# Kernel optimization log

Hardware: AMD Instinct MI355X
Metric: run time of the kernel (lower is better)

Reference implementation:

```python
import jax, jax.numpy as jnp
import numpy as np

B, S, D, H, HD = 8, 1374, 384, 6, 64
NUM_PATCHES = 1369  # (518 // 14) ** 2
NUM_PREFIX = 5      # 1 cls + 4 registers


def setup_inputs() -> dict:
    key = jax.random.key(0)
    ks = jax.random.split(key, 10)
    init = 0.02  # truncated_normal(0.02) approximated by scaled normal
    x = jax.random.normal(ks[0], (B, S, D), jnp.float32)
    wq = jax.random.truncated_normal(ks[1], -2.0, 2.0, (D, H, HD), jnp.float32) * init
    wk = jax.random.truncated_normal(ks[2], -2.0, 2.0, (D, H, HD), jnp.float32) * init
    wv = jax.random.truncated_normal(ks[3], -2.0, 2.0, (D, H, HD), jnp.float32) * init
    wo = jax.random.truncated_normal(ks[4], -2.0, 2.0, (H, HD, D), jnp.float32) * init
    bq = jnp.zeros((H, HD), jnp.float32)
    bk = jnp.zeros((H, HD), jnp.float32)
    bv = jnp.zeros((H, HD), jnp.float32)
    bo = jnp.zeros((D,), jnp.float32)
    keep_patch_indices = jax.random.randint(ks[5], (B, NUM_PATCHES), 0, NUM_PATCHES).astype(jnp.int64)
    return {"x": x, "wq": wq, "bq": bq, "wk": wk, "bk": bk, "wv": wv, "bv": bv,
            "wo": wo, "bo": bo, "keep_patch_indices": keep_patch_indices, "k_patches": 685}


def reference(x, wq, bq, wk, bk, wv, bv, wo, bo, keep_patch_indices, k_patches):
    # q/k/v projections: DenseGeneral to (heads, head_dim)
    q = jnp.einsum('bsd,dhe->bshe', x, wq) + bq
    k = jnp.einsum('bsd,dhe->bshe', x, wk) + bk
    v = jnp.einsum('bsd,dhe->bshe', x, wv) + bv

    z = jnp.einsum('bqhd,bkhd->bhqk', q / (HD ** 0.5), k)  # [B,H,S,S]
    attn_logits = z  # saved BEFORE masking (used by 'mse' criterion)

    # dynamic scatter mask: patch columns >= k_patches get -inf
    num_selected = keep_patch_indices.shape[1]
    patch_idx = jnp.arange(num_selected)
    indices_to_mask = jnp.where(patch_idx >= k_patches, patch_idx, num_selected) + NUM_PREFIX
    # out-of-bounds indices (== num_selected + NUM_PREFIX) are dropped by JAX scatter semantics
    z = z.at[:, :, :, indices_to_mask].set(-jnp.inf)

    attn_map = jax.nn.softmax(z, axis=-1)
    zo = jnp.einsum('bhqk,bkhd->bqhd', attn_map, v)
    output = jnp.einsum('bqhd,hdo->bqo', zo, wo) + bo  # wo contracts (heads, head_dim)

    # attn_aggregate = ['cls_token','reg_token','patch_token'], zoom_map_criterion='mse'
    am = attn_logits.mean(axis=1)  # mean over heads -> [B,S,S]
    aggs = jnp.stack([
        am[:, 0:1, :].mean(axis=1),      # cls token
        am[:, 1:5, :].mean(axis=1),      # register tokens
        am[:, 5:1374, :].mean(axis=1),   # patch tokens
    ], axis=1)                            # [B,3,S]
    attn_agg = aggs.mean(axis=1)          # [B,S]
    return output, attn_agg
```

## Files before the change

### kernel.cpp

```cpp
#include <hip/hip_runtime.h>
#include <stdint.h>

#define BB 8
#define SS 1374
#define DD 384
#define HH 6
#define HDIM 64
#define MROWS (BB*SS)
#define NPFX 5
#define SPAD 1376

typedef __attribute__((ext_vector_type(8))) short bf16x8;
typedef __attribute__((ext_vector_type(4))) float f32x4;
typedef __attribute__((ext_vector_type(2))) unsigned int u32x2;
typedef __attribute__((ext_vector_type(4))) unsigned int u32x4;
typedef u32x4 __attribute__((aligned(4))) u32x4_u;

__device__ __forceinline__ unsigned short f2bf(float f){
  union { float f; unsigned int u; } v; v.f = f;
  return (unsigned short)((v.u + 0x7FFFu + ((v.u >> 16) & 1u)) >> 16);
}
__device__ __forceinline__ float bf2f(unsigned short b){
  union { float f; unsigned int u; } v; v.u = ((unsigned int)b) << 16; return v.f;
}
__device__ __forceinline__ unsigned int pk_bf16(float a, float b){
#if __has_builtin(__builtin_amdgcn_cvt_pk_bf16_f32)
  typedef __attribute__((ext_vector_type(2))) __bf16 bfv2;
  bfv2 p = __builtin_amdgcn_cvt_pk_bf16_f32(a, b);
  union { bfv2 v; unsigned int u; } c; c.v = p; return c.u;
#else
  return (unsigned int)f2bf(a) | ((unsigned int)f2bf(b) << 16);
#endif
}

__global__ void k_prep_x(const float* __restrict__ x, unsigned short* __restrict__ xb,
                         float* __restrict__ xbar){
  int b = blockIdx.x / 43, ch = blockIdx.x % 43;
  int d = threadIdx.x;
  int s0 = ch*32, s1 = s0 + 32; if (s1 > SS) s1 = SS;
  float acc = 0.f;
  for (int s = s0; s < s1; ++s){
    float v = x[((size_t)b*SS + s)*DD + d];
    float w = (s == 0) ? (1.f/3.f) : (s < 5) ? (1.f/12.f) : (1.f/4107.f);
    acc += w * v;
    xb[((size_t)b*SS + s)*DD + d] = f2bf(v);
  }
  atomicAdd(&xbar[b*DD + d], acc);
}

__global__ void k_conv_w(const float* __restrict__ wq, const float* __restrict__ wk,
                         const float* __restrict__ wv, const float* __restrict__ wo,
                         unsigned short* __restrict__ wbT, unsigned short* __restrict__ woT){
  int i = blockIdx.x*blockDim.x + threadIdx.x;
  if (i < 1152*384){
    int n = i / 384, d = i % 384;
    const float* w = (n < 384) ? wq : (n < 768) ? wk : wv;
    wbT[i] = f2bf(w[(size_t)d*384 + (n % 384)]);
  } else if (i < 1152*384 + 384*384){
    int j = i - 1152*384;
    int n = j / 384, k = j % 384;
    woT[j] = f2bf(wo[(size_t)k*384 + n]);
  }
}

__global__ void k_qbar(const float* __restrict__ xbar, const float* __restrict__ wq,
                       const float* __restrict__ bq, float* __restrict__ qbar){
  __shared__ float xs[DD];
  int b = blockIdx.x, t = threadIdx.x;
  xs[t] = xbar[b*DD + t];
  __syncthreads();
  float acc = bq[t];
  for (int d = 0; d < DD; ++d) acc += xs[d]*wq[(size_t)d*384 + t];
  qbar[b*384 + t] = acc;
}

__global__ void k_agg(const float* __restrict__ qbar, const unsigned short* __restrict__ kg,
                      float* __restrict__ out_agg){
  __shared__ float qs[384];
  int b = blockIdx.x / 6, sb = blockIdx.x % 6;
  int t = threadIdx.x;
  for (int i = t; i < 384; i += 256) qs[i] = qbar[b*384 + i];
  __syncthreads();
  int s = sb*256 + t;
  if (s >= SS) return;
  float acc = 0.f;
  for (int h = 0; h < HH; ++h){
    const unsigned short* kr = kg + (((size_t)(b*HH + h))*SS + s)*64;
    const float* qh = qs + h*64;
    for (int c = 0; c < 8; ++c){
      u32x4 v = *(const u32x4*)(kr + c*8);
      #pragma unroll
      for (int j = 0; j < 4; ++j){
        unsigned int u = v[j];
        acc += qh[c*8 + 2*j]     * bf2f((unsigned short)(u & 0xFFFFu));
        acc += qh[c*8 + 2*j + 1] * bf2f((unsigned short)(u >> 16));
      }
    }
  }
  out_agg[b*SS + s] = acc * (1.f/48.f);
}

template<int MODE>
__global__ __launch_bounds__(256) void k_gemm(
    const unsigned short* __restrict__ A, const unsigned short* __restrict__ Bt,
    const float* __restrict__ b0, const float* __restrict__ b1, const float* __restrict__ b2,
    unsigned short* __restrict__ qg, unsigned short* __restrict__ kgp,
    unsigned short* __restrict__ vt, float* __restrict__ out)
{
  int mt = blockIdx.x % 86, nt = blockIdx.x / 86;
  const int t = threadIdx.x;
  const int w = t >> 6, lane = t & 63, quad = lane >> 4, l16 = lane & 15;
  const int wm = w >> 1, wn = w & 1;
  constexpr int SMEM_SH = (MODE==0) ? 13824 : 17408;
  __shared__ unsigned short smem[SMEM_SH];
  unsigned short* As = smem;
  unsigned short* Bs = smem + 9216;
  f32x4 acc[4][2];
  #pragma unroll
  for (int i=0;i<4;i++){ acc[i][0] = (f32x4){0,0,0,0}; acc[i][1] = (f32x4){0,0,0,0}; }
  const int m0 = mt*128, n0 = nt*64;

  const int ar = t >> 1, akb = (t & 1) * 32;
  int ga = m0 + ar; if (ga > MROWS-1) ga = MROWS-1;
  const unsigned short* ap = A + (size_t)ga*384 + akb;
  const int br = t >> 2, bkb = (t & 3) * 16;
  const unsigned short* bp = Bt + (size_t)(n0 + br)*384 + bkb;

  u32x4 ra[4], rb[2];
  #pragma unroll
  for (int i=0;i<4;i++) ra[i] = *(const u32x4*)(ap + i*8);
  rb[0] = *(const u32x4*)(bp); rb[1] = *(const u32x4*)(bp + 8);

  for (int kc = 0; kc < 6; ++kc){
    __syncthreads();
    #pragma unroll
    for (int i=0;i<4;i++) *(u32x4*)(As + ar*72 + akb + i*8) = ra[i];
    *(u32x4*)(Bs + br*72 + bkb)     = rb[0];
    *(u32x4*)(Bs + br*72 + bkb + 8) = rb[1];
    __syncthreads();
    if (kc + 1 < 6){
      int kn = (kc+1)*64;
      #pragma unroll
      for (int i=0;i<4;i++) ra[i] = *(const u32x4*)(ap + kn + i*8);
      rb[0] = *(const u32x4*)(bp + kn); rb[1] = *(const u32x4*)(bp + kn + 8);
    }
    #pragma unroll
    for (int kh = 0; kh < 2; ++kh){
      bf16x8 af[4], bfr[2];
      #pragma unroll
      for (int rf = 0; rf < 4; ++rf)
        af[rf] = *(const bf16x8*)(As + (wm*64 + rf*16 + l16)*72 + kh*32 + quad*8);
      #pragma unroll
      for (int cf = 0; cf < 2; ++cf)
        bfr[cf] = *(const bf16x8*)(Bs + (wn*32 + cf*16 + l16)*72 + kh*32 + quad*8);
      #pragma unroll
      for (int rf = 0; rf < 4; ++rf)
        #pragma unroll
        for (int cf = 0; cf < 2; ++cf)
          acc[rf][cf] = __builtin_amdgcn_mfma_f32_16x16x32_bf16(af[rf], bfr[cf], acc[rf][cf], 0,0,0);
    }
  }

  const int b0r = m0 / SS, s0r = m0 % SS;
  __syncthreads();
  if (MODE == 1){
    float* CsF = (float*)smem;
    #pragma unroll
    for (int cf = 0; cf < 2; ++cf){
      int e = wn*32 + cf*16 + l16;
      float bias = b0[n0 + e];
      #pragma unroll
      for (int rf = 0; rf < 4; ++rf){
        int rr = wm*64 + rf*16 + quad*4;
        #pragma unroll
        for (int r4 = 0; r4 < 4; ++r4)
          CsF[(rr + r4)*68 + e] = acc[rf][cf][r4] + bias;
      }
    }
    __syncthreads();
    #pragma unroll
    for (int p = 0; p < 8; ++p){
      int r = p*16 + (t >> 4), c = t & 15;
      int rr = m0 + r;
      if (rr < MROWS){
        f32x4 v = *(const f32x4*)(CsF + r*68 + c*4);
        *(f32x4*)(out + (size_t)rr*384 + n0 + c*4) = v;
      }
    }
  } else {
    const int mat = nt / 6, h = nt - mat*6;
    const float* bvp = (mat==0) ? b0 : (mat==1) ? b1 : b2;
    const float vsc = (mat==0) ? 0.125f : 1.f;
    if (mat < 2){
      unsigned short* Cs = As;
      unsigned short* dst = (mat==0) ? qg : kgp;
      #pragma unroll
      for (int cf = 0; cf < 2; ++cf){
        int e = wn*32 + cf*16 + l16;
        float bias = bvp[h*64 + e];
        #pragma unroll
        for (int rf = 0; rf < 4; ++rf){
          int rr = wm*64 + rf*16 + quad*4;
          #pragma unroll
          for (int r4 = 0; r4 < 4; ++r4)
            Cs[(rr + r4)*72 + e] = f2bf((acc[rf][cf][r4] + bias)*vsc);
        }
      }
      __syncthreads();
      #pragma unroll
      for (int p = 0; p < 4; ++p){
        int r = p*32 + (t >> 3), c = t & 7;
        int rr = m0 + r;
        if (rr < MROWS){
          int s = s0r + r, bb = b0r;
          if (s >= SS){ s -= SS; ++bb; }
          u32x4 v = *(const u32x4*)(Cs + r*72 + c*8);
          *(u32x4*)(dst + (((size_t)(bb*HH + h))*SS + s)*64 + c*8) = v;
        }
      }
    } else {
      unsigned short* CsV = As;
      #pragma unroll
      for (int cf = 0; cf < 2; ++cf){
        int e = wn*32 + cf*16 + l16;
        float bias = bvp[h*64 + e];
        #pragma unroll
        for (int rf = 0; rf < 4; ++rf){
          int rr = wm*64 + rf*16 + quad*4;
          #pragma unroll
          for (int p = 0; p < 2; ++p)
            *(unsigned int*)(CsV + e*136 + rr + p*2) =
                pk_bf16(acc[rf][cf][p*2] + bias, acc[rf][cf][p*2+1] + bias);
        }
      }
      __syncthreads();
      const bool nowrap = (s0r + 127 < SS) && (m0 + 127 < MROWS);
      if (nowrap){
        int e = t >> 2;
        unsigned short* vrow = vt + ((size_t)(b0r*HH + h)*64 + e)*SPAD + s0r;
        #pragma unroll
        for (int i = 0; i < 4; ++i){
          int c = (t & 3)*4 + i;
          u32x4 v = *(const u32x4*)(CsV + e*136 + c*8);
          *(u32x4_u*)(vrow + c*8) = v;
        }
      } else {
        for (int idx = t; idx < 64*64; idx += 256){
          int e = idx >> 6, sp = (idx & 63)*2;
          int rr = m0 + sp;
          if (rr < MROWS){
            int s = s0r + sp, bb = b0r;
            if (s >= SS){ s -= SS; ++bb; }
            *(unsigned int*)(vt + ((size_t)(bb*HH + h)*64 + e)*SPAD + s) =
                *(const unsigned int*)(CsV + e*136 + sp);
          }
        }
      }
    }
  }
}

__global__ __launch_bounds__(128) void k_attn(
    const unsigned short* __restrict__ qg, const unsigned short* __restrict__ kg,
    const unsigned short* __restrict__ vt, unsigned short* __restrict__ zo,
    const int* __restrict__ kpat)
{
  int t = threadIdx.x, w = t >> 6, lane = t & 63, quad = lane >> 4, l16 = lane & 15;
  int wid = blockIdx.x*2 + w;
  int bh = wid / 43, qt = wid - bh*43;
  int q0 = qt*32;
  int SK = NPFX + kpat[0]; if (SK > SS) SK = SS; if (SK < 1) SK = 1;
  int niter = (SK + 63) >> 6;
  __shared__ unsigned short Ps[2][32*72];
  unsigned short* Pw = &Ps[w][0];
  const unsigned short* kbase = kg + ((size_t)bh*SS)*64;
  const unsigned short* vbase = vt + ((size_t)bh*64)*SPAD;

  bf16x8 aq[2][2];
  #pragma unroll
  for (int qf = 0; qf < 2; ++qf){
    int qrow = q0 + qf*16 + l16; if (qrow > SS-1) qrow = SS-1;
    const unsigned short* p = qg + ((size_t)bh*SS + qrow)*64;
    aq[qf][0] = *(const bf16x8*)(p + quad*8);
    aq[qf][1] = *(const bf16x8*)(p + 32 + quad*8);
  }
  f32x4 o[2][4];
  #pragma unroll
  for (int qf=0;qf<2;qf++)
    #pragma unroll
    for (int nc=0;nc<4;nc++) o[qf][nc] = (f32x4){0.f,0.f,0.f,0.f};
  float rsum[2][4] = {{0.f,0.f,0.f,0.f},{0.f,0.f,0.f,0.f}};

  auto loadK = [&](int k0, bf16x8 (&kf)[2][2][2]){
    #pragma unroll
    for (int ks = 0; ks < 2; ++ks)
      #pragma unroll
      for (int ns = 0; ns < 2; ++ns){
        const unsigned short* kr = kbase + (size_t)(k0 + ks*32 + 2*l16 + ns)*64;
        kf[ks][ns][0] = *(const bf16x8*)(kr + quad*8);
        kf[ks][ns][1] = *(const bf16x8*)(kr + 32 + quad*8);
      }
  };

  auto body = [&](int it, bf16x8 (&kfC)[2][2][2], bf16x8 (&kfN)[2][2][2]){
    int k0 = it*64;
    bf16x8 vf[2][4];
    #pragma unroll
    for (int kc = 0; kc < 2; ++kc)
      #pragma unroll
      for (int nc = 0; nc < 4; ++nc)
        vf[kc][nc] = *(const bf16x8*)(vbase + (size_t)(nc*16 + l16)*SPAD + k0 + kc*32 + quad*8);
    if (it + 1 < niter) loadK(k0 + 64, kfN);
    bool tail = (k0 + 64 > SK);
    #pragma unroll
    for (int ks = 0; ks < 2; ++ks){
      #pragma unroll
      for (int qf = 0; qf < 2; ++qf){
        float pp[2][4];
        #pragma unroll
        for (int ns = 0; ns < 2; ++ns){
          f32x4 zf = (f32x4){0.f,0.f,0.f,0.f};
          zf = __builtin_amdgcn_mfma_f32_16x16x32_bf16(aq[qf][0], kfC[ks][ns][0], zf, 0,0,0);
          zf = __builtin_amdgcn_mfma_f32_16x16x32_bf16(aq[qf][1], kfC[ks][ns][1], zf, 0,0,0);
          bool valid = !tail || (k0 + ks*32 + 2*l16 + ns) < SK;
          #pragma unroll
          for (int rg = 0; rg < 4; ++rg) pp[ns][rg] = valid ? __expf(zf[rg]) : 0.f;
        }
        #pragma unroll
        for (int rg = 0; rg < 4; ++rg){
          rsum[qf][rg] += pp[0][rg] + pp[1][rg];
          *(unsigned int*)(Pw + (qf*16 + quad*4 + rg)*72 + ks*32 + 2*l16) =
              pk_bf16(pp[0][rg], pp[1][rg]);
        }
      }
    }
    #pragma unroll
    for (int kc = 0; kc < 2; ++kc){
      bf16x8 ap0 = *(const bf16x8*)(Pw + l16*72        + kc*32 + quad*8);
      bf16x8 ap1 = *(const bf16x8*)(Pw + (16 + l16)*72 + kc*32 + quad*8);
      #pragma unroll
      for (int nc = 0; nc < 4; ++nc){
        o[0][nc] = __builtin_amdgcn_mfma_f32_16x16x32_bf16(ap0, vf[kc][nc], o[0][nc], 0,0,0);
        o[1][nc] = __builtin_amdgcn_mfma_f32_16x16x32_bf16(ap1, vf[kc][nc], o[1][nc], 0,0,0);
      }
    }
  };

  bf16x8 kfA[2][2][2], kfB[2][2][2];
  loadK(0, kfA);
  for (int it = 0; it < niter; it += 2){
    body(it, kfA, kfB);
    if (it + 1 < niter) body(it + 1, kfB, kfA);
  }

  int b = bh / HH, h = bh - (bh/HH)*HH;
  #pragma unroll
  for (int qf = 0; qf < 2; ++qf){
    #pragma unroll
    for (int rg = 0; rg < 4; ++rg){
      float s = rsum[qf][rg];
      #pragma unroll
      for (int off = 8; off >= 1; off >>= 1) s += __shfl_xor(s, off);
      int q = q0 + qf*16 + quad*4 + rg;
      if (q >= SS) continue;
      float inv = 1.f / s;
      unsigned short* dst = zo + ((size_t)b*SS + q)*384 + h*64;
      #pragma unroll
      for (int nc = 0; nc < 4; ++nc) dst[nc*16 + l16] = f2bf(o[qf][nc][rg]*inv);
    }
  }
}

extern "C" void kernel_launch(void* const* d_in, const int* in_sizes, int n_in,
                              void* d_out, int out_size, void* d_ws, size_t ws_size,
                              hipStream_t stream){
  const float* x  = (const float*)d_in[0];
  const float* wq = (const float*)d_in[1];
  const float* bq = (const float*)d_in[2];
  const float* wk = (const float*)d_in[3];
  const float* bk = (const float*)d_in[4];
  const float* wv = (const float*)d_in[5];
  const float* bv = (const float*)d_in[6];
  const float* wo = (const float*)d_in[7];
  const float* bo = (const float*)d_in[8];
  const int* kpat = (const int*)d_in[10];
  float* out = (float*)d_out;
  float* out_agg = out + (size_t)MROWS*DD;

  char* ws = (char*)d_ws;
  unsigned short* xb  = (unsigned short*)(ws);
  unsigned short* wbT = (unsigned short*)(ws +  8441856);
  unsigned short* woT = (unsigned short*)(ws +  9326592);
  unsigned short* qg  = (unsigned short*)(ws +  9621504);
  unsigned short* kg  = (unsigned short*)(ws + 18063360);
  unsigned short* vt  = (unsigned short*)(ws + 26505216);
  unsigned short* zo  = (unsigned short*)(ws + 34959360);
  float* xbar         = (float*)(ws + 43401216);
  float* qbar         = (float*)(ws + 43413504);
  (void)in_sizes; (void)n_in; (void)out_size; (void)ws_size;

  hipMemsetAsync(xbar, 0, BB*DD*sizeof(float), stream);
  k_prep_x<<<BB*43, DD, 0, stream>>>(x, xb, xbar);
  k_conv_w<<<((1152*384 + 384*384) + 255)/256, 256, 0, stream>>>(wq, wk, wv, wo, wbT, woT);
  k_qbar<<<BB, DD, 0, stream>>>(xbar, wq, bq, qbar);
  k_gemm<0><<<86*18, 256, 0, stream>>>(xb, wbT, bq, bk, bv, qg, kg, vt, nullptr);
  k_attn<<<1032, 128, 0, stream>>>(qg, kg, vt, zo, kpat);
  k_agg<<<BB*6, 256, 0, stream>>>(qbar, kg, out_agg);
  k_gemm<1><<<86*6, 256, 0, stream>>>(zo, woT, bo, nullptr, nullptr, nullptr, nullptr, nullptr, out);
}
```

Baseline: 198.3 us.

## Split attention key loop across four waves per query tile with LDS reduction

Each query tile now gets a 256-thread block, and its four waves take interleaved 64-key chunks instead of one wave walking all keys. The K prefetch stride is adjusted to match. Partial output accumulators and row sums are combined through shared memory, with one wave normalising and storing each 16-row half. This quadruples the number of waves so more latency can be hidden and more SIMDs kept busy. In exchange it adds LDS traffic, three block barriers and per-wave Q-fragment reloads.

```diff
diff --git a/kernel.cpp b/kernel.cpp
--- a/kernel.cpp
+++ b/kernel.cpp
@@ -260,18 +260,19 @@
   }
 }
 
-__global__ __launch_bounds__(128) void k_attn(
+__global__ __launch_bounds__(256) void k_attn(
     const unsigned short* __restrict__ qg, const unsigned short* __restrict__ kg,
     const unsigned short* __restrict__ vt, unsigned short* __restrict__ zo,
     const int* __restrict__ kpat)
 {
   int t = threadIdx.x, w = t >> 6, lane = t & 63, quad = lane >> 4, l16 = lane & 15;
-  int wid = blockIdx.x*2 + w;
-  int bh = wid / 43, qt = wid - bh*43;
+  int blk = blockIdx.x;
+  int bh = blk / 43, qt = blk - bh*43;
   int q0 = qt*32;
   int SK = NPFX + kpat[0]; if (SK > SS) SK = SS; if (SK < 1) SK = 1;
   int niter = (SK + 63) >> 6;
-  __shared__ unsigned short Ps[2][32*72];
+  __shared__ unsigned short Ps[4][32*72];
+  __shared__ float Rs[4][64][20];
   unsigned short* Pw = &Ps[w][0];
   const unsigned short* kbase = kg + ((size_t)bh*SS)*64;
   const unsigned short* vbase = vt + ((size_t)bh*64)*SPAD;
@@ -310,7 +311,7 @@
       #pragma unroll
       for (int nc = 0; nc < 4; ++nc)
         vf[kc][nc] = *(const bf16x8*)(vbase + (size_t)(nc*16 + l16)*SPAD + k0 + kc*32 + quad*8);
-    if (it + 1 < niter) loadK(k0 + 64, kfN);
+    if (it + 4 < niter) loadK(k0 + 256, kfN);
     bool tail = (k0 + 64 > SK);
     #pragma unroll
     for (int ks = 0; ks < 2; ++ks){
@@ -347,18 +348,31 @@
   };
 
   bf16x8 kfA[2][2][2], kfB[2][2][2];
-  loadK(0, kfA);
-  for (int it = 0; it < niter; it += 2){
-    body(it, kfA, kfB);
-    if (it + 1 < niter) body(it + 1, kfB, kfA);
-  }
-
-  int b = bh / HH, h = bh - (bh/HH)*HH;
-  #pragma unroll
-  for (int qf = 0; qf < 2; ++qf){
+  if (w < niter) loadK(w*64, kfA);
+  int parity = 0;
+  for (int it = w; it < niter; it += 4, parity ^= 1){
+    if (parity == 0) body(it, kfA, kfB); else body(it, kfB, kfA);
+  }
+
+  const int b = bh / HH, h = bh - (bh/HH)*HH;
+  auto reduceStore = [&](int qf){
+    f32x4 oo[4]; float rr[4];
+    #pragma unroll
+    for (int nc=0;nc<4;nc++) oo[nc] = (f32x4){0.f,0.f,0.f,0.f};
+    rr[0]=rr[1]=rr[2]=rr[3]=0.f;
+    #pragma unroll
+    for (int v = 0; v < 4; ++v){
+      #pragma unroll
+      for (int nc = 0; nc < 4; ++nc){
+        f32x4 x = *(const f32x4*)&Rs[v][lane][nc*4];
+        oo[nc] += x;
+      }
+      f32x4 r = *(const f32x4*)&Rs[v][lane][16];
+      rr[0] += r[0]; rr[1] += r[1]; rr[2] += r[2]; rr[3] += r[3];
+    }
     #pragma unroll
     for (int rg = 0; rg < 4; ++rg){
-      float s = rsum[qf][rg];
+      float s = rr[rg];
       #pragma unroll
       for (int off = 8; off >= 1; off >>= 1) s += __shfl_xor(s, off);
       int q = q0 + qf*16 + quad*4 + rg;
@@ -366,9 +380,21 @@
       float inv = 1.f / s;
       unsigned short* dst = zo + ((size_t)b*SS + q)*384 + h*64;
       #pragma unroll
-      for (int nc = 0; nc < 4; ++nc) dst[nc*16 + l16] = f2bf(o[qf][nc][rg]*inv);
-    }
-  }
+      for (int nc = 0; nc < 4; ++nc) dst[nc*16 + l16] = f2bf(oo[nc][rg]*inv);
+    }
+  };
+
+  #pragma unroll
+  for (int nc = 0; nc < 4; ++nc) *(f32x4*)&Rs[w][lane][nc*4] = o[0][nc];
+  { f32x4 r = {rsum[0][0], rsum[0][1], rsum[0][2], rsum[0][3]}; *(f32x4*)&Rs[w][lane][16] = r; }
+  __syncthreads();
+  if (w == 0) reduceStore(0);
+  __syncthreads();
+  #pragma unroll
+  for (int nc = 0; nc < 4; ++nc) *(f32x4*)&Rs[w][lane][nc*4] = o[1][nc];
+  { f32x4 r = {rsum[1][0], rsum[1][1], rsum[1][2], rsum[1][3]}; *(f32x4*)&Rs[w][lane][16] = r; }
+  __syncthreads();
+  if (w == 1) reduceStore(1);
 }
 
 extern "C" void kernel_launch(void* const* d_in, const int* in_sizes, int n_in,
@@ -404,7 +430,7 @@
   k_conv_w<<<((1152*384 + 384*384) + 255)/256, 256, 0, stream>>>(wq, wk, wv, wo, wbT, woT);
   k_qbar<<<BB, DD, 0, stream>>>(xbar, wq, bq, qbar);
   k_gemm<0><<<86*18, 256, 0, stream>>>(xb, wbT, bq, bk, bv, qg, kg, vt, nullptr);
-  k_attn<<<1032, 128, 0, stream>>>(qg, kg, vt, zo, kpat);
+  k_attn<<<2064, 256, 0, stream>>>(qg, kg, vt, zo, kpat);
   k_agg<<<BB*6, 256, 0, stream>>>(qbar, kg, out_agg);
   k_gemm<1><<<86*6, 256, 0, stream>>>(zo, woT, bo, nullptr, nullptr, nullptr, nullptr, nullptr, out);
 }
```

Measured after the change: 230.0 us. 16.0% more time.
